# Optimization experiments

Hardware: AMD Instinct MI355X
Metric: run time of the kernel (lower is better)

## Reference

```python
import jax, jax.numpy as jnp
import numpy as np

N_NODES = 100000
N_EDGES = 1600000
LATENT = 64
NODE_DIM = 7
EDGE_DIM = 3
N_PARAMS = 2

def asinh_layer(p, x):
    # learned asinh: a*arcsinh(b*x + c) + d, p = [a, b, c, d]
    return p[0] * jnp.arcsinh(p[1] * x + p[2]) + p[3]

def mlp2(x, w1, b1, w2, b2):
    # ExplicitMLP([L, L]): gelu between layers, none on last
    return jax.nn.gelu(x @ w1 + b1) @ w2 + b2

def agg_stats(x, n):
    # custom_aggregation: [sum, mean, var, max]; mean/var denominators are n_data
    s = jnp.sum(x, axis=0, keepdims=True)
    m = s / n
    v = jnp.sum((x - m) ** 2, axis=0, keepdims=True) / n
    mx = jnp.max(x, axis=0, keepdims=True)
    return jnp.concatenate([s, m, v, mx], axis=-1)

def _forward(nodes, edges, asinh_node, w_en, b_en, asinh_edge, w_ee, b_ee, asinh_glob, w_eg, b_eg, ew1, eb1, ew2, eb2, nw1, nb1, nw2, nb2, gw1, gb1, gw2, gb2, gw3, gb3, senders):
    # decorate_nodes=False -> zero columns 0:4
    nodes = nodes.at[:, 0:4].set(0.0)
    # globals = arcsinh([n_node, n_edge]) as (1, 2)
    glob = jnp.arcsinh(jnp.array([[float(N_NODES), float(N_EDGES)]], dtype=nodes.dtype))
    # GraphMapFeatures embedding: asinh layer + Dense for nodes/edges/globals
    nodes = asinh_layer(asinh_node, nodes) @ w_en + b_en   # (N, L)
    edges = asinh_layer(asinh_edge, edges) @ w_ee + b_ee   # (E, L)
    glob = asinh_layer(asinh_glob, glob) @ w_eg + b_eg     # (1, L)
    # source overwrites receivers with senders
    recv = senders
    # edge update: concat(edges, nodes[senders], nodes[receivers], globals)
    ge = jnp.broadcast_to(glob, (edges.shape[0], glob.shape[-1]))
    e_in = jnp.concatenate([edges, nodes[senders], nodes[recv], ge], axis=-1)  # (E, 4L)
    edges = mlp2(e_in, ew1, eb1, ew2, eb2)                                     # (E, L)
    # node update: sent/received aggregates are identical since recv == senders
    sent = jax.ops.segment_sum(edges, senders, num_segments=N_NODES)           # (N, L)
    gn = jnp.broadcast_to(glob, (nodes.shape[0], glob.shape[-1]))
    n_in = jnp.concatenate([nodes, sent, sent, gn], axis=-1)                   # (N, 4L)
    nodes = mlp2(n_in, nw1, nb1, nw2, nb2)                                     # (N, L)
    # global update: arcsinh of [sum, mean, var, max] over nodes and edges (single graph)
    node_attr = jnp.arcsinh(agg_stats(nodes, float(N_NODES)))                  # (1, 4L)
    edge_attr = jnp.arcsinh(agg_stats(edges, float(N_EDGES)))                  # (1, 4L)
    g_in = jnp.concatenate([node_attr, edge_attr, glob], axis=-1)              # (1, 9L)
    g = jax.nn.gelu(g_in @ gw1 + gb1)
    g = jax.nn.gelu(g @ gw2 + gb2)
    g = g @ gw3 + gb3
    return g.reshape(-1)  # (N_PARAMS,)

def setup_inputs():
    key = jax.random.key(0)
    ks = jax.random.split(key, 16)
    L = LATENT
    def dense(k, fi, fo):
        return jax.random.normal(k, (fi, fo), jnp.float32) / np.float32(np.sqrt(fi))
    z = lambda n: jnp.zeros((n,), jnp.float32)
    asinh0 = jnp.array([1.0, 1.0, 0.0, 0.0], jnp.float32)
    return {
        "nodes": jax.random.normal(ks[0], (N_NODES, NODE_DIM), jnp.float32),
        "edges": jax.random.normal(ks[1], (N_EDGES, EDGE_DIM), jnp.float32),
        "senders": jax.random.randint(ks[2], (N_EDGES,), 0, N_NODES),
        "asinh_node": asinh0, "w_en": dense(ks[3], NODE_DIM, L), "b_en": z(L),
        "asinh_edge": asinh0, "w_ee": dense(ks[4], EDGE_DIM, L), "b_ee": z(L),
        "asinh_glob": asinh0, "w_eg": dense(ks[5], 2, L), "b_eg": z(L),
        "ew1": dense(ks[6], 4 * L, L), "eb1": z(L),
        "ew2": dense(ks[7], L, L), "eb2": z(L),
        "nw1": dense(ks[8], 4 * L, L), "nb1": z(L),
        "nw2": dense(ks[9], L, L), "nb2": z(L),
        "gw1": dense(ks[10], 9 * L, L), "gb1": z(L),
        "gw2": dense(ks[11], L, L), "gb2": z(L),
        "gw3": dense(ks[12], L, N_PARAMS), "gb3": z(N_PARAMS),
    }

def reference(nodes, edges, senders, asinh_node, w_en, b_en, asinh_edge, w_ee, b_ee, asinh_glob, w_eg, b_eg, ew1, eb1, ew2, eb2, nw1, nb1, nw2, nb2, gw1, gb1, gw2, gb2, gw3, gb3):
    return _forward(nodes, edges, asinh_node, w_en, b_en, asinh_edge, w_ee, b_ee, asinh_glob, w_eg, b_eg, ew1, eb1, ew2, eb2, nw1, nb1, nw2, nb2, gw1, gb1, gw2, gb2, gw3, gb3, senders)
```

## Files before the change

kernel.cpp:

```cpp
#include <hip/hip_runtime.h>
#include <cstdint>
#include <cstddef>

#define NN 100000
#define NE 1600000
#define NSLICE 16
#define NBLK 782
#define NBUCK 391
#define CHA 4096
#define CAPB 6144

#define PRE_GLOB 0
#define PRE_WC   64
#define PRE_CVEC 256
#define PRE_CN   320
#define PRE_NGV  384
#define PRE_WSR  448
#define PRE_NSR  4544

#define TAB_W2  0
#define TAB_NW1 1
#define TAB_NSR 2
#define TAB_NW2 3
#define TAB_WSR 4

typedef short v8s __attribute__((ext_vector_type(8)));
typedef float v4f __attribute__((ext_vector_type(4)));

__device__ __forceinline__ float asinhf_fast(float x){
    float ax = fabsf(x);
    float r = __logf(ax + sqrtf(fmaf(ax, ax, 1.0f)));
    return copysignf(r, x);
}
__device__ __forceinline__ float gelu_f(float x){
    float x3 = x * x * x;
    float y = 1.5957691216057308f * fmaf(0.044715f, x3, x);
    float e = __expf(y);
    float r = __builtin_amdgcn_rcpf(e + 1.0f);
    return fmaf(-x, r, x);
}
__device__ __forceinline__ unsigned fkey(float f){
    unsigned u = __float_as_uint(f);
    return (u & 0x80000000u) ? ~u : (u | 0x80000000u);
}
__device__ __forceinline__ float funkey(unsigned k){
    unsigned u = (k & 0x80000000u) ? (k ^ 0x80000000u) : ~k;
    return __uint_as_float(u);
}
__device__ __forceinline__ void atomAddF(float* p, float v){
#if defined(__HIP_DEVICE_COMPILE__)
    unsafeAtomicAdd(p, v);
#else
    atomicAdd(p, v);
#endif
}
__device__ __forceinline__ void split8(const float* x, v8s& hi, v8s& lo){
#pragma unroll
    for (int j = 0; j < 8; ++j){
        unsigned u = __float_as_uint(x[j]);
        float hf = __uint_as_float(u & 0xFFFF0000u);
        float r = x[j] - hf;
        hi[j] = (short)(u >> 16);
        lo[j] = (short)(__float_as_uint(r) >> 16);
    }
}
__device__ __forceinline__ v4f mfma3(v8s ah, v8s al, v8s bh, v8s bl, v4f acc){
    acc = __builtin_amdgcn_mfma_f32_16x16x32_bf16(al, bh, acc, 0, 0, 0);
    acc = __builtin_amdgcn_mfma_f32_16x16x32_bf16(ah, bl, acc, 0, 0, 0);
    acc = __builtin_amdgcn_mfma_f32_16x16x32_bf16(ah, bh, acc, 0, 0, 0);
    return acc;
}
__device__ __forceinline__ void fma16(float acc[4][4], float4 a, float4 b){
    float av[4] = {a.x, a.y, a.z, a.w};
    float bv[4] = {b.x, b.y, b.z, b.w};
#pragma unroll
    for (int i = 0; i < 4; ++i)
#pragma unroll
        for (int c = 0; c < 4; ++c)
            acc[i][c] = fmaf(av[i], bv[c], acc[i][c]);
}

__global__ __launch_bounds__(256) void k_pre(const float* an, const float* w_en, const float* b_en,
                      const float* ae, const float* w_ee, const float* b_ee,
                      const float* ag, const float* w_eg, const float* b_eg,
                      const float* ew1, const float* eb1,
                      const float* nw1, const float* nb1,
                      const float* ew2, const float* nw2,
                      float* pre, unsigned short* preB, int* statsZero, int* counts)
{
    __shared__ float gls[64];
    __shared__ float red[3][4][64];
    __shared__ float redc[4][64], redn[4][64];
    int t = threadIdx.x, col = t & 63, qd = t >> 6;
    for (int i = t; i < 2 * NSLICE * 192; i += 256) statsZero[i] = 0;
    {
        int4* c4 = (int4*)counts;
        int4 z = make_int4(0, 0, 0, 0);
        for (int i = t; i < NN / 4; i += 256) c4[i] = z;
    }
    for (int i = t; i < 4096; i += 256){
        pre[PRE_WSR + i] = ew1[4096 + i] + ew1[8192 + i];
        pre[PRE_NSR + i] = nw1[4096 + i] + nw1[8192 + i];
    }
    if (t < 64){
        float g0 = asinhf_fast(100000.0f);
        float g1 = asinhf_fast(1600000.0f);
        float tg0 = fmaf(ag[0], asinhf_fast(fmaf(ag[1], g0, ag[2])), ag[3]);
        float tg1 = fmaf(ag[0], asinhf_fast(fmaf(ag[1], g1, ag[2])), ag[3]);
        float gl = fmaf(tg0, w_eg[t], fmaf(tg1, w_eg[64 + t], b_eg[t]));
        pre[PRE_GLOB + t] = gl;
        gls[t] = gl;
        float tz = fmaf(an[0], asinhf_fast(an[2]), an[3]);
        pre[PRE_CN + t] = fmaf(tz, w_en[t] + w_en[64 + t] + w_en[128 + t] + w_en[192 + t], b_en[t]);
    }
    __syncthreads();
    {
        float s0 = 0.f, s1 = 0.f, s2 = 0.f, sc = 0.f, sn = 0.f;
        int jb = qd * 16;
#pragma unroll 4
        for (int j = jb; j < jb + 16; ++j){
            float e1 = ew1[j * 64 + col];
            s0 = fmaf(w_ee[j], e1, s0);
            s1 = fmaf(w_ee[64 + j], e1, s1);
            s2 = fmaf(w_ee[128 + j], e1, s2);
            sc = fmaf(b_ee[j], e1, sc);
            float g = gls[j];
            sc = fmaf(g, ew1[(192 + j) * 64 + col], sc);
            sn = fmaf(g, nw1[(192 + j) * 64 + col], sn);
        }
        red[0][qd][col] = s0; red[1][qd][col] = s1; red[2][qd][col] = s2;
        redc[qd][col] = sc; redn[qd][col] = sn;
    }
    __syncthreads();
    if (t < 64){
#pragma unroll
        for (int i = 0; i < 3; ++i)
            pre[PRE_WC + i * 64 + t] = (red[i][0][t] + red[i][1][t]) + (red[i][2][t] + red[i][3][t]);
        pre[PRE_CVEC + t] = eb1[t] + (redc[0][t] + redc[1][t]) + (redc[2][t] + redc[3][t]);
        pre[PRE_NGV + t] = nb1[t] + (redn[0][t] + redn[1][t]) + (redn[2][t] + redn[3][t]);
    }
    __syncthreads();
    const float* srcs[5] = {ew2, nw1, pre + PRE_NSR, nw2, pre + PRE_WSR};
    for (int idx = t; idx < 5 * 4096; idx += 256){
        int tab = idx >> 12;
        int rem = idx & 4095;
        int c = rem >> 10;
        int ch = (rem >> 9) & 1;
        int lane = (rem >> 3) & 63;
        int j = rem & 7;
        int k = ch * 32 + (lane >> 4) * 8 + j;
        int n = c * 16 + (lane & 15);
        float v = srcs[tab][k * 64 + n];
        unsigned u = __float_as_uint(v);
        float hf = __uint_as_float(u & 0xFFFF0000u);
        float r = v - hf;
        int base = tab * 8192 + ((c * 2 + ch) * 2) * 512 + lane * 8 + j;
        preB[base] = (unsigned short)(u >> 16);
        preB[base + 512] = (unsigned short)(__float_as_uint(r) >> 16);
    }
}

__global__ __launch_bounds__(256) void k_nproj(const float* nodes, const float* an,
                                               const float* w_en, const float* pre,
                                               const unsigned short* preB,
                                               const int* senders, int* counts,
                                               float* lat, float* nproj)
{
    __shared__ float fz[64][4];
    __shared__ float latS[64][68];
    int t = threadIdx.x;
    int base = blockIdx.x * 64;
    int cnt = NN - base; if (cnt > 64) cnt = 64;
    {
        const int NT = 1563 * 256;
        for (int i = blockIdx.x * 256 + t; i < NE; i += NT)
            atomicAdd(&counts[senders[i]], 1);
    }
    if (t < 64){
        float pa = an[0], pb = an[1], pc = an[2], pd = an[3];
        int n = base + t;
        float t4 = 0.f, t5 = 0.f, t6 = 0.f;
        if (t < cnt){
            const float* row = nodes + (size_t)n * 7;
            t4 = fmaf(pa, asinhf_fast(fmaf(pb, row[4], pc)), pd);
            t5 = fmaf(pa, asinhf_fast(fmaf(pb, row[5], pc)), pd);
            t6 = fmaf(pa, asinhf_fast(fmaf(pb, row[6], pc)), pd);
        }
        fz[t][0] = t4; fz[t][1] = t5; fz[t][2] = t6;
    }
    __syncthreads();
    {
        int k = t & 63, grp = t >> 6;
        float w4 = w_en[4 * 64 + k], w5 = w_en[5 * 64 + k], w6 = w_en[6 * 64 + k];
        float cn = pre[PRE_CN + k];
#pragma unroll
        for (int i = 0; i < 16; ++i){
            int nl = grp * 16 + i;
            float v = 0.f;
            if (nl < cnt){
                v = cn;
                v = fmaf(fz[nl][0], w4, v);
                v = fmaf(fz[nl][1], w5, v);
                v = fmaf(fz[nl][2], w6, v);
                lat[(size_t)(base + nl) * 64 + k] = v;
            }
            latS[nl][k] = v;
        }
    }
    __syncthreads();
    int l = t & 63, w = t >> 6;
    int m = l & 15, q = l >> 4;
    v8s ah[2], al[2];
#pragma unroll
    for (int ch = 0; ch < 2; ++ch){
        float a[8];
        const float* src = &latS[w * 16 + m][ch * 32 + q * 8];
#pragma unroll
        for (int j = 0; j < 8; ++j) a[j] = src[j];
        split8(a, ah[ch], al[ch]);
    }
    const v8s* WB = (const v8s*)(preB + TAB_WSR * 8192);
    v4f acc[4];
#pragma unroll
    for (int c = 0; c < 4; ++c){
        acc[c] = (v4f){0.f, 0.f, 0.f, 0.f};
#pragma unroll
        for (int ch = 0; ch < 2; ++ch){
            v8s bh = WB[((c * 2 + ch) * 2 + 0) * 64 + l];
            v8s bl = WB[((c * 2 + ch) * 2 + 1) * 64 + l];
            acc[c] = mfma3(ah[ch], al[ch], bh, bl, acc[c]);
        }
    }
#pragma unroll
    for (int c = 0; c < 4; ++c)
#pragma unroll
        for (int r = 0; r < 4; ++r){
            int nl = w * 16 + q * 4 + r;
            if (nl < cnt)
                nproj[(size_t)(base + nl) * 64 + c * 16 + m] = acc[c][r];
        }
}

__global__ __launch_bounds__(128) void k_scanA(const int* counts, int* cursor, int* bsums)
{
    __shared__ int sA[128];
    int t = threadIdx.x, b = blockIdx.x;
    int i = b * 128 + t;
    int v = (i < NN) ? counts[i] : 0;
    sA[t] = v;
    __syncthreads();
    for (int off = 1; off < 128; off <<= 1){
        int x = (t >= off) ? sA[t - off] : 0;
        __syncthreads();
        sA[t] += x;
        __syncthreads();
    }
    if (i < NN) cursor[i] = sA[t] - v;
    if (t == 127) bsums[b] = sA[127];
}

__global__ __launch_bounds__(1024) void k_scanB(const int* bsums, int* bpre, int* bucketFill)
{
    __shared__ int sB[1024];
    int t = threadIdx.x;
    int v = (t < NBLK) ? bsums[t] : 0;
    sB[t] = v;
    __syncthreads();
    for (int off = 1; off < 1024; off <<= 1){
        int x = (t >= off) ? sB[t - off] : 0;
        __syncthreads();
        sB[t] += x;
        __syncthreads();
    }
    if (t < NBLK) bpre[t] = sB[t] - v;
    if (t < NBUCK) bucketFill[t] = (t == 0) ? 0 : sB[2 * t - 1];
}

__global__ __launch_bounds__(256) void k_binA(const int* senders, int* bucketFill, int* binned)
{
    __shared__ int hist[NBUCK], hist2[NBUCK], runS[NBUCK];
    __shared__ int lofs[NBUCK + 1];
    __shared__ int sA[512];
    __shared__ int staged[CHA];
    int t = threadIdx.x, b = blockIdx.x;
    int beg = b * CHA;
    int end = beg + CHA; if (end > NE) end = NE;
    int n = end - beg;
    for (int i = t; i < NBUCK; i += 256){ hist[i] = 0; hist2[i] = 0; }
    __syncthreads();
    for (int i = beg + t; i < end; i += 256)
        atomicAdd(&hist[senders[i] >> 8], 1);
    __syncthreads();
    sA[t] = (t < NBUCK) ? hist[t] : 0;
    sA[t + 256] = (t + 256 < NBUCK) ? hist[t + 256] : 0;
    __syncthreads();
    for (int off = 1; off < 512; off <<= 1){
        int x0 = (t >= off) ? sA[t - off] : 0;
        int p = t + 256;
        int x1 = (p >= off) ? sA[p - off] : 0;
        __syncthreads();
        sA[t] += x0; sA[p] += x1;
        __syncthreads();
    }
    if (t < NBUCK) lofs[t] = sA[t] - hist[t];
    if (t + 256 < NBUCK) lofs[t + 256] = sA[t + 256] - hist[t + 256];
    if (t == 0) lofs[NBUCK] = n;
    for (int i = t; i < NBUCK; i += 256)
        if (hist[i] > 0) runS[i] = atomicAdd(&bucketFill[i], hist[i]);
    __syncthreads();
    for (int i = beg + t; i < end; i += 256){
        int bk = senders[i] >> 8;
        int r = atomicAdd(&hist2[bk], 1);
        staged[lofs[bk] + r] = i;
    }
    __syncthreads();
    for (int p = t; p < n; p += 256){
        int lo = 0, hi = NBUCK;
        while (hi - lo > 1){
            int mid = (lo + hi) >> 1;
            if (lofs[mid] <= p) lo = mid; else hi = mid;
        }
        binned[runS[lo] + (p - lofs[lo])] = staged[p];
    }
}

__global__ __launch_bounds__(256) void k_binB(const int* binned, const int* senders,
                                              const int* cursor, const int* bpre, int* perm)
{
    __shared__ int cnt256[256];
    __shared__ int staged[CAPB];
    int t = threadIdx.x, b = blockIdx.x;
    int base = bpre[2 * b];
    int end = (b == NBUCK - 1) ? NE : bpre[2 * b + 2];
    int cnt = end - base;
    cnt256[t] = 0;
    __syncthreads();
    if (cnt <= CAPB){
        for (int i = base + t; i < end; i += 256){
            int idx = binned[i];
            int s = senders[idx];
            int r = atomicAdd(&cnt256[s & 255], 1);
            int pos = cursor[s] + bpre[s >> 7] + r;
            staged[pos - base] = idx;
        }
        __syncthreads();
        for (int i = t; i < cnt; i += 256) perm[base + i] = staged[i];
    } else {
        for (int i = base + t; i < end; i += 256){
            int idx = binned[i];
            int s = senders[idx];
            int r = atomicAdd(&cnt256[s & 255], 1);
            perm[cursor[s] + bpre[s >> 7] + r] = idx;
        }
    }
}

__global__ __launch_bounds__(256) void k_edge_sorted(const int* perm, const int* senders,
                                                     const float* edges, const float* nproj,
                                                     const float* pre, const unsigned short* preB,
                                                     const float* ae, const float* eb2,
                                                     float* sent, float* epart)
{
    __shared__ float oS[64][65];
    __shared__ float cWs[256];
    __shared__ int sArr[64];
    int t = threadIdx.x;
    cWs[t] = (t < 64) ? pre[PRE_CVEC + t] : pre[PRE_WC + t - 64];
    int l = t & 63, w = t >> 6;
    int m = l & 15, q = l >> 4;
    int e = w * 16 + m;
    int idx = perm[blockIdx.x * 64 + e];
    int s = senders[idx];
    if (q == 0) sArr[e] = s;
    const float* er = edges + (size_t)idx * 3;
    float f0 = er[0], f1 = er[1], f2 = er[2];
    const float4* npb = (const float4*)(nproj + (size_t)s * 64);
    float4 npv0 = npb[2 * q], npv1 = npb[2 * q + 1];
    float4 npv2 = npb[8 + 2 * q], npv3 = npb[8 + 2 * q + 1];
    float pa = ae[0], pb = ae[1], pc = ae[2], pd = ae[3];
    float t0 = fmaf(pa, asinhf_fast(fmaf(pb, f0, pc)), pd);
    float t1 = fmaf(pa, asinhf_fast(fmaf(pb, f1, pc)), pd);
    float t2 = fmaf(pa, asinhf_fast(fmaf(pb, f2, pc)), pd);
    __syncthreads();
    float npf[2][8] = {{npv0.x, npv0.y, npv0.z, npv0.w, npv1.x, npv1.y, npv1.z, npv1.w},
                       {npv2.x, npv2.y, npv2.z, npv2.w, npv3.x, npv3.y, npv3.z, npv3.w}};
    v8s ah[2], al[2];
#pragma unroll
    for (int ch = 0; ch < 2; ++ch){
        int k0 = ch * 32 + q * 8;
        float h[8];
#pragma unroll
        for (int j = 0; j < 8; ++j){
            int k = k0 + j;
            float hp = cWs[k] + npf[ch][j];
            hp = fmaf(t0, cWs[64 + k], hp);
            hp = fmaf(t1, cWs[128 + k], hp);
            hp = fmaf(t2, cWs[192 + k], hp);
            h[j] = gelu_f(hp);
        }
        split8(h, ah[ch], al[ch]);
    }
    const v8s* WB = (const v8s*)(preB + TAB_W2 * 8192);
#pragma unroll
    for (int c = 0; c < 4; ++c){
        v4f acc = (v4f){0.f, 0.f, 0.f, 0.f};
#pragma unroll
        for (int ch = 0; ch < 2; ++ch){
            v8s bh = WB[((c * 2 + ch) * 2 + 0) * 64 + l];
            v8s bl = WB[((c * 2 + ch) * 2 + 1) * 64 + l];
            acc = mfma3(ah[ch], al[ch], bh, bl, acc);
        }
        float bb = eb2[c * 16 + m];
#pragma unroll
        for (int r = 0; r < 4; ++r)
            oS[w * 16 + q * 4 + r][c * 16 + m] = acc[r] + bb;
    }
    __syncthreads();
    if (w == 0){
        int k = l;
        int cur = sArr[0];
        int jstart = 0;
        float a = 0.f;
        for (int j = 0; j < 64; ++j){
            int sj = sArr[j];
            if (sj != cur){
                float* dst = sent + (size_t)cur * 64 + k;
                if (jstart > 0) *dst = a; else atomAddF(dst, a);
                cur = sj; a = 0.f; jstart = j;
            }
            a += oS[j][k];
        }
        atomAddF(sent + (size_t)cur * 64 + k, a);
    } else if (w == 1){
        int k = l;
        float ssum = 0.f, qsum = 0.f, mmax = -INFINITY;
#pragma unroll 4
        for (int j = 0; j < 64; ++j){
            float v = oS[j][k];
            ssum += v;
            qsum = fmaf(v, v, qsum);
            mmax = fmaxf(mmax, v);
        }
        float* ep = epart + (size_t)(blockIdx.x & (NSLICE - 1)) * 192;
        atomAddF(ep + k, ssum);
        atomAddF(ep + 64 + k, qsum);
        atomicMax((unsigned*)(ep + 128) + k, fkey(mmax));
    }
}

__global__ __launch_bounds__(256) void k_edge_atomic(const float* edges, const int* senders,
                                                     const float* nproj, const float* pre,
                                                     const float* ae, const float* ew2, const float* eb2,
                                                     float* sent, float* epart)
{
    __shared__ float hT[64][68];
    __shared__ int sArr[64];
    int t = threadIdx.x;
    int e = t & 63, kq = t >> 6;
    int eg = blockIdx.x * 64 + e;
    int s = senders[eg];
    if (kq == 0) sArr[e] = s;
    float pa = ae[0], pb = ae[1], pc = ae[2], pd = ae[3];
    const float* erow = edges + (size_t)eg * 3;
    float t0 = fmaf(pa, asinhf_fast(fmaf(pb, erow[0], pc)), pd);
    float t1 = fmaf(pa, asinhf_fast(fmaf(pb, erow[1], pc)), pd);
    float t2 = fmaf(pa, asinhf_fast(fmaf(pb, erow[2], pc)), pd);
    int j0 = kq * 16;
    const float* np = nproj + (size_t)s * 64 + j0;
    float npv[16];
#pragma unroll
    for (int qq = 0; qq < 4; ++qq){
        float4 v = *(const float4*)(np + qq * 4);
        npv[qq * 4 + 0] = v.x; npv[qq * 4 + 1] = v.y; npv[qq * 4 + 2] = v.z; npv[qq * 4 + 3] = v.w;
    }
    const float* Wc = pre + PRE_WC;
    const float* cvec = pre + PRE_CVEC;
#pragma unroll
    for (int jj = 0; jj < 16; ++jj){
        int j = j0 + jj;
        float hp = cvec[j] + npv[jj];
        hp = fmaf(t0, Wc[j], hp);
        hp = fmaf(t1, Wc[64 + j], hp);
        hp = fmaf(t2, Wc[128 + j], hp);
        hT[j][e] = gelu_f(hp);
    }
    __syncthreads();
    int e0 = (t & 15) * 4, k0 = (t >> 4) * 4;
    float acc[4][4];
    {
        float4 bb = *(const float4*)(eb2 + k0);
#pragma unroll
        for (int i = 0; i < 4; ++i){ acc[i][0] = bb.x; acc[i][1] = bb.y; acc[i][2] = bb.z; acc[i][3] = bb.w; }
    }
#pragma unroll 4
    for (int j = 0; j < 64; ++j){
        float4 a = *(const float4*)&hT[j][e0];
        float4 b = *(const float4*)(ew2 + j * 64 + k0);
        fma16(acc, a, b);
    }
#pragma unroll
    for (int i = 0; i < 4; ++i){
        int sv = sArr[e0 + i];
        float* dst = sent + (size_t)sv * 64 + k0;
        atomAddF(dst + 0, acc[i][0]);
        atomAddF(dst + 1, acc[i][1]);
        atomAddF(dst + 2, acc[i][2]);
        atomAddF(dst + 3, acc[i][3]);
    }
    float ps[4], pq[4], pm[4];
#pragma unroll
    for (int c = 0; c < 4; ++c){
        float s0 = acc[0][c], s1 = acc[1][c], s2 = acc[2][c], s3 = acc[3][c];
        ps[c] = (s0 + s1) + (s2 + s3);
        pq[c] = fmaf(s0, s0, fmaf(s1, s1, fmaf(s2, s2, s3 * s3)));
        pm[c] = fmaxf(fmaxf(s0, s1), fmaxf(s2, s3));
    }
#pragma unroll
    for (int msk = 1; msk < 16; msk <<= 1){
#pragma unroll
        for (int c = 0; c < 4; ++c){
            ps[c] += __shfl_xor(ps[c], msk);
            pq[c] += __shfl_xor(pq[c], msk);
            pm[c] = fmaxf(pm[c], __shfl_xor(pm[c], msk));
        }
    }
    float* ep = epart + (size_t)(blockIdx.x & (NSLICE - 1)) * 192;
    if ((t & 15) == 0){
#pragma unroll
        for (int c = 0; c < 4; ++c){
            atomAddF(ep + k0 + c, ps[c]);
            atomAddF(ep + 64 + k0 + c, pq[c]);
            atomicMax((unsigned*)(ep + 128) + k0 + c, fkey(pm[c]));
        }
    }
}

__global__ __launch_bounds__(256) void k_node(const float* lat, const float* sent, const float* pre,
                                              const unsigned short* preB, const float* nb2,
                                              float* npart)
{
    __shared__ float h2S[64][68];
    __shared__ float sS[4][64], qS[4][64], mS[4][64];
    int t = threadIdx.x;
    int base = blockIdx.x * 64;
    int cnt = NN - base; if (cnt > 64) cnt = 64;
    int l = t & 63, w = t >> 6;
    int m = l & 15, q = l >> 4;
    int rowA = w * 16 + m;
    bool vA = rowA < cnt;
    v8s lh[2], ll[2], sh[2], sl[2];
#pragma unroll
    for (int ch = 0; ch < 2; ++ch){
        float a[8] = {0,0,0,0,0,0,0,0}, b[8] = {0,0,0,0,0,0,0,0};
        if (vA){
            const float4* pl = (const float4*)(lat + (size_t)(base + rowA) * 64 + ch * 32 + q * 8);
            const float4* psn = (const float4*)(sent + (size_t)(base + rowA) * 64 + ch * 32 + q * 8);
            float4 a0 = pl[0], a1 = pl[1], b0 = psn[0], b1 = psn[1];
            a[0]=a0.x; a[1]=a0.y; a[2]=a0.z; a[3]=a0.w; a[4]=a1.x; a[5]=a1.y; a[6]=a1.z; a[7]=a1.w;
            b[0]=b0.x; b[1]=b0.y; b[2]=b0.z; b[3]=b0.w; b[4]=b1.x; b[5]=b1.y; b[6]=b1.z; b[7]=b1.w;
        }
        split8(a, lh[ch], ll[ch]);
        split8(b, sh[ch], sl[ch]);
    }
    const v8s* B1 = (const v8s*)(preB + TAB_NW1 * 8192);
    const v8s* BS = (const v8s*)(preB + TAB_NSR * 8192);
    v4f acc[4];
#pragma unroll
    for (int c = 0; c < 4; ++c){
        acc[c] = (v4f){0.f, 0.f, 0.f, 0.f};
#pragma unroll
        for (int ch = 0; ch < 2; ++ch){
            v8s bh = B1[((c * 2 + ch) * 2 + 0) * 64 + l];
            v8s bl = B1[((c * 2 + ch) * 2 + 1) * 64 + l];
            acc[c] = mfma3(lh[ch], ll[ch], bh, bl, acc[c]);
            v8s ch2 = BS[((c * 2 + ch) * 2 + 0) * 64 + l];
            v8s cl2 = BS[((c * 2 + ch) * 2 + 1) * 64 + l];
            acc[c] = mfma3(sh[ch], sl[ch], ch2, cl2, acc[c]);
        }
        float g = pre[PRE_NGV + c * 16 + m];
#pragma unroll
        for (int r = 0; r < 4; ++r)
            h2S[w * 16 + q * 4 + r][c * 16 + m] = gelu_f(acc[c][r] + g);
    }
    __syncthreads();
    v8s ah[2], al[2];
#pragma unroll
    for (int ch = 0; ch < 2; ++ch){
        float a[8];
        const float* src = &h2S[w * 16 + m][ch * 32 + q * 8];
#pragma unroll
        for (int j = 0; j < 8; ++j) a[j] = src[j];
        split8(a, ah[ch], al[ch]);
    }
    const v8s* B2 = (const v8s*)(preB + TAB_NW2 * 8192);
    float ps[4], pq[4], pm[4];
#pragma unroll
    for (int c = 0; c < 4; ++c){
        v4f a2 = (v4f){0.f, 0.f, 0.f, 0.f};
#pragma unroll
        for (int ch = 0; ch < 2; ++ch){
            v8s bh = B2[((c * 2 + ch) * 2 + 0) * 64 + l];
            v8s bl = B2[((c * 2 + ch) * 2 + 1) * 64 + l];
            a2 = mfma3(ah[ch], al[ch], bh, bl, a2);
        }
        float bb = nb2[c * 16 + m];
        ps[c] = 0.f; pq[c] = 0.f; pm[c] = -INFINITY;
#pragma unroll
        for (int r = 0; r < 4; ++r){
            int nl = w * 16 + q * 4 + r;
            if (nl < cnt){
                float v = a2[r] + bb;
                ps[c] += v;
                pq[c] = fmaf(v, v, pq[c]);
                pm[c] = fmaxf(pm[c], v);
            }
        }
    }
#pragma unroll
    for (int msk = 16; msk <= 32; msk <<= 1){
#pragma unroll
        for (int c = 0; c < 4; ++c){
            ps[c] += __shfl_xor(ps[c], msk);
            pq[c] += __shfl_xor(pq[c], msk);
            pm[c] = fmaxf(pm[c], __shfl_xor(pm[c], msk));
        }
    }
    if (l < 16){
#pragma unroll
        for (int c = 0; c < 4; ++c){
            sS[w][c * 16 + l] = ps[c];
            qS[w][c * 16 + l] = pq[c];
            mS[w][c * 16 + l] = pm[c];
        }
    }
    __syncthreads();
    if (t < 64){
        int k = t;
        float ssum = sS[0][k] + sS[1][k] + sS[2][k] + sS[3][k];
        float qsum = qS[0][k] + qS[1][k] + qS[2][k] + qS[3][k];
        float mmax = fmaxf(fmaxf(mS[0][k], mS[1][k]), fmaxf(mS[2][k], mS[3][k]));
        float* np = npart + (size_t)(blockIdx.x & (NSLICE - 1)) * 192;
        atomAddF(np + k, ssum);
        atomAddF(np + 64 + k, qsum);
        atomicMax((unsigned*)(np + 128) + k, fkey(mmax));
    }
}

__global__ __launch_bounds__(256) void k_final(const float* pre, const float* epart, const float* npart,
                        const float* gw1, const float* gb1, const float* gw2, const float* gb2,
                        const float* gw3, const float* gb3, float* out)
{
    __shared__ float gin[576];
    __shared__ float p1[4][64];
    __shared__ float l1s[64];
    __shared__ float l2s[64];
    int t = threadIdx.x;
    if (t < 64){
        float ns = 0.f, nq = 0.f; unsigned nmk = 0u;
        float es = 0.f, eq = 0.f; unsigned emk = 0u;
        for (int sl = 0; sl < NSLICE; ++sl){
            const float* np = npart + (size_t)sl * 192;
            const float* ep = epart + (size_t)sl * 192;
            ns += np[t]; nq += np[64 + t];
            unsigned a = ((const unsigned*)(np + 128))[t]; if (a > nmk) nmk = a;
            es += ep[t]; eq += ep[64 + t];
            unsigned b = ((const unsigned*)(ep + 128))[t]; if (b > emk) emk = b;
        }
        float mean = ns / 100000.0f;
        float var = nq / 100000.0f - mean * mean;
        gin[t] = asinhf_fast(ns);
        gin[64 + t] = asinhf_fast(mean);
        gin[128 + t] = asinhf_fast(var);
        gin[192 + t] = asinhf_fast(funkey(nmk));
        float meane = es / 1600000.0f;
        float vare = eq / 1600000.0f - meane * meane;
        gin[256 + t] = asinhf_fast(es);
        gin[320 + t] = asinhf_fast(meane);
        gin[384 + t] = asinhf_fast(vare);
        gin[448 + t] = asinhf_fast(funkey(emk));
        gin[512 + t] = pre[PRE_GLOB + t];
    }
    __syncthreads();
    {
        int col = t & 63, qq = t >> 6;
        float a1 = 0.f;
        for (int j = qq * 144; j < qq * 144 + 144; ++j)
            a1 = fmaf(gin[j], gw1[j * 64 + col], a1);
        p1[qq][col] = a1;
    }
    __syncthreads();
    if (t < 64){
        float a = gb1[t] + ((p1[0][t] + p1[1][t]) + (p1[2][t] + p1[3][t]));
        l1s[t] = gelu_f(a);
    }
    __syncthreads();
    if (t < 64){
        float a2 = gb2[t];
        for (int j = 0; j < 64; ++j) a2 = fmaf(l1s[j], gw2[j * 64 + t], a2);
        l2s[t] = gelu_f(a2);
    }
    __syncthreads();
    if (t < 2){
        float s = gb3[t];
        for (int j = 0; j < 64; ++j) s = fmaf(l2s[j], gw3[j * 2 + t], s);
        out[t] = s;
    }
}

extern "C" void kernel_launch(void* const* d_in, const int* in_sizes, int n_in,
                              void* d_out, int out_size, void* d_ws, size_t ws_size,
                              hipStream_t stream)
{
    const float* nodes  = (const float*)d_in[0];
    const float* edges  = (const float*)d_in[1];
    const int*   senders= (const int*)d_in[2];
    const float* an  = (const float*)d_in[3];
    const float* w_en= (const float*)d_in[4];
    const float* b_en= (const float*)d_in[5];
    const float* ae  = (const float*)d_in[6];
    const float* w_ee= (const float*)d_in[7];
    const float* b_ee= (const float*)d_in[8];
    const float* ag  = (const float*)d_in[9];
    const float* w_eg= (const float*)d_in[10];
    const float* b_eg= (const float*)d_in[11];
    const float* ew1 = (const float*)d_in[12];
    const float* eb1 = (const float*)d_in[13];
    const float* ew2 = (const float*)d_in[14];
    const float* eb2 = (const float*)d_in[15];
    const float* nw1 = (const float*)d_in[16];
    const float* nb1 = (const float*)d_in[17];
    const float* nw2 = (const float*)d_in[18];
    const float* nb2 = (const float*)d_in[19];
    const float* gw1 = (const float*)d_in[20];
    const float* gb1 = (const float*)d_in[21];
    const float* gw2 = (const float*)d_in[22];
    const float* gb2 = (const float*)d_in[23];
    const float* gw3 = (const float*)d_in[24];
    const float* gb3 = (const float*)d_in[25];

    char* ws = (char*)d_ws;
    float*  lat   = (float*)(ws);
    float*  nproj = (float*)(ws + 25600000);
    float*  sent  = (float*)(ws + 51200000);
    float*  pre   = (float*)(ws + 76800000);
    unsigned short* preB = (unsigned short*)(ws + 76865536);
    float*  epart = (float*)(ws + 76963840);
    float*  npart = (float*)(ws + 76976128);
    int*    counts= (int*)  (ws + 77000000);
    int*    cursor= (int*)  (ws + 77400000);
    int*    bsums = (int*)  (ws + 77800000);
    int*    bpre  = (int*)  (ws + 77804096);
    int*    perm  = (int*)  (ws + 77810000);
    int*    binned= (int*)  (ws + 84210000);
    int*    bucketFill = (int*)(ws + 90610000);

    const size_t NEED_FAST = 90620000;
    bool fast = (ws_size >= NEED_FAST);

    hipMemsetAsync(sent, 0, (size_t)NN * 64 * sizeof(float), stream);

    hipLaunchKernelGGL(k_pre, dim3(1), dim3(256), 0, stream,
                       an, w_en, b_en, ae, w_ee, b_ee, ag, w_eg, b_eg, ew1, eb1,
                       nw1, nb1, ew2, nw2, pre, preB, (int*)epart, counts);

    if (fast){
        hipLaunchKernelGGL(k_nproj, dim3((NN + 63) / 64), dim3(256), 0, stream,
                           nodes, an, w_en, pre, preB, senders, counts, lat, nproj);
        hipLaunchKernelGGL(k_scanA, dim3(NBLK), dim3(128), 0, stream, counts, cursor, bsums);
        hipLaunchKernelGGL(k_scanB, dim3(1), dim3(1024), 0, stream, bsums, bpre, bucketFill);
        hipLaunchKernelGGL(k_binA, dim3(NBUCK), dim3(256), 0, stream, senders, bucketFill, binned);
        hipLaunchKernelGGL(k_binB, dim3(NBUCK), dim3(256), 0, stream,
                           binned, senders, cursor, bpre, perm);
        hipLaunchKernelGGL(k_edge_sorted, dim3(NE / 64), dim3(256), 0, stream,
                           perm, senders, edges, nproj, pre, preB, ae, eb2, sent, epart);
    } else {
        hipLaunchKernelGGL(k_nproj, dim3((NN + 63) / 64), dim3(256), 0, stream,
                           nodes, an, w_en, pre, preB, senders, cursor, lat, nproj);
        hipLaunchKernelGGL(k_edge_atomic, dim3(NE / 64), dim3(256), 0, stream,
                           edges, senders, nproj, pre, ae, ew2, eb2, sent, epart);
    }

    hipLaunchKernelGGL(k_node, dim3((NN + 63) / 64), dim3(256), 0, stream,
                       lat, sent, pre, preB, nb2, npart);
    hipLaunchKernelGGL(k_final, dim3(1), dim3(256), 0, stream,
                       pre, epart, npart, gw1, gb1, gw2, gb2, gw3, gb3, (float*)d_out);
}
```

Before: 437.2 us.

## Carry transformed edge features through binning and recompute node latents in node kernel

The binning passes now move packed float4 records holding the three asinh-transformed edge features plus the sender id, instead of edge indices. This removes the perm gather, the senders lookup and the random edge-row reads from the edge kernel. The lat buffer is dropped and node latents are recomputed from the raw node rows inside k_node, and the memset of sent is folded into k_nproj as a grid-stride zero loop. In exchange, binned traffic is four times wider, the workspace requirement grows, and binB loses its shared-memory staging, so its scattered writes now go straight to global memory.

```diff
diff --git a/kernel.cpp b/kernel.cpp
--- a/kernel.cpp
+++ b/kernel.cpp
@@ -7,8 +7,8 @@
 #define NSLICE 16
 #define NBLK 782
 #define NBUCK 391
+#define NCHUNK 391
 #define CHA 4096
-#define CAPB 6144
 
 #define PRE_GLOB 0
 #define PRE_WC   64
@@ -164,24 +164,27 @@
                                                const float* w_en, const float* pre,
                                                const unsigned short* preB,
                                                const int* senders, int* counts,
-                                               float* lat, float* nproj)
+                                               float* sent, float* nproj)
 {
     __shared__ float fz[64][4];
     __shared__ float latS[64][68];
     int t = threadIdx.x;
     int base = blockIdx.x * 64;
     int cnt = NN - base; if (cnt > 64) cnt = 64;
+    const int NT = 1563 * 256;
+    int gtid = blockIdx.x * 256 + t;
+    for (int i = gtid; i < NE; i += NT)
+        atomicAdd(&counts[senders[i]], 1);
     {
-        const int NT = 1563 * 256;
-        for (int i = blockIdx.x * 256 + t; i < NE; i += NT)
-            atomicAdd(&counts[senders[i]], 1);
+        float4 z = make_float4(0.f, 0.f, 0.f, 0.f);
+        float4* s4 = (float4*)sent;
+        for (int i = gtid; i < NN * 16; i += NT) s4[i] = z;
     }
     if (t < 64){
         float pa = an[0], pb = an[1], pc = an[2], pd = an[3];
-        int n = base + t;
         float t4 = 0.f, t5 = 0.f, t6 = 0.f;
         if (t < cnt){
-            const float* row = nodes + (size_t)n * 7;
+            const float* row = nodes + (size_t)(base + t) * 7;
             t4 = fmaf(pa, asinhf_fast(fmaf(pb, row[4], pc)), pd);
             t5 = fmaf(pa, asinhf_fast(fmaf(pb, row[5], pc)), pd);
             t6 = fmaf(pa, asinhf_fast(fmaf(pb, row[6], pc)), pd);
@@ -196,15 +199,11 @@
 #pragma unroll
         for (int i = 0; i < 16; ++i){
             int nl = grp * 16 + i;
-            float v = 0.f;
-            if (nl < cnt){
-                v = cn;
-                v = fmaf(fz[nl][0], w4, v);
-                v = fmaf(fz[nl][1], w5, v);
-                v = fmaf(fz[nl][2], w6, v);
-                lat[(size_t)(base + nl) * 64 + k] = v;
-            }
-            latS[nl][k] = v;
+            float v = cn;
+            v = fmaf(fz[nl][0], w4, v);
+            v = fmaf(fz[nl][1], w5, v);
+            v = fmaf(fz[nl][2], w6, v);
+            latS[nl][k] = (nl < cnt) ? v : 0.f;
         }
     }
     __syncthreads();
@@ -276,7 +275,8 @@
     if (t < NBUCK) bucketFill[t] = (t == 0) ? 0 : sB[2 * t - 1];
 }
 
-__global__ __launch_bounds__(256) void k_binA(const int* senders, int* bucketFill, int* binned)
+__global__ __launch_bounds__(256) void k_binA(const float* edges, const int* senders,
+                                              const float* ae, int* bucketFill, float4* binned)
 {
     __shared__ int hist[NBUCK], hist2[NBUCK], runS[NBUCK];
     __shared__ int lofs[NBUCK + 1];
@@ -314,51 +314,43 @@
         staged[lofs[bk] + r] = i;
     }
     __syncthreads();
+    float pa = ae[0], pb = ae[1], pc = ae[2], pd = ae[3];
     for (int p = t; p < n; p += 256){
         int lo = 0, hi = NBUCK;
         while (hi - lo > 1){
             int mid = (lo + hi) >> 1;
             if (lofs[mid] <= p) lo = mid; else hi = mid;
         }
-        binned[runS[lo] + (p - lofs[lo])] = staged[p];
-    }
-}
-
-__global__ __launch_bounds__(256) void k_binB(const int* binned, const int* senders,
-                                              const int* cursor, const int* bpre, int* perm)
+        int idx = staged[p];
+        const float* er = edges + (size_t)idx * 3;
+        float t0 = fmaf(pa, asinhf_fast(fmaf(pb, er[0], pc)), pd);
+        float t1 = fmaf(pa, asinhf_fast(fmaf(pb, er[1], pc)), pd);
+        float t2 = fmaf(pa, asinhf_fast(fmaf(pb, er[2], pc)), pd);
+        binned[runS[lo] + (p - lofs[lo])] =
+            make_float4(t0, t1, t2, __int_as_float(senders[idx]));
+    }
+}
+
+__global__ __launch_bounds__(256) void k_binB(const float4* binned, const int* cursor,
+                                              const int* bpre, float4* eperm)
 {
     __shared__ int cnt256[256];
-    __shared__ int staged[CAPB];
     int t = threadIdx.x, b = blockIdx.x;
     int base = bpre[2 * b];
     int end = (b == NBUCK - 1) ? NE : bpre[2 * b + 2];
-    int cnt = end - base;
     cnt256[t] = 0;
     __syncthreads();
-    if (cnt <= CAPB){
-        for (int i = base + t; i < end; i += 256){
-            int idx = binned[i];
-            int s = senders[idx];
-            int r = atomicAdd(&cnt256[s & 255], 1);
-            int pos = cursor[s] + bpre[s >> 7] + r;
-            staged[pos - base] = idx;
-        }
-        __syncthreads();
-        for (int i = t; i < cnt; i += 256) perm[base + i] = staged[i];
-    } else {
-        for (int i = base + t; i < end; i += 256){
-            int idx = binned[i];
-            int s = senders[idx];
-            int r = atomicAdd(&cnt256[s & 255], 1);
-            perm[cursor[s] + bpre[s >> 7] + r] = idx;
-        }
-    }
-}
-
-__global__ __launch_bounds__(256) void k_edge_sorted(const int* perm, const int* senders,
-                                                     const float* edges, const float* nproj,
+    for (int i = base + t; i < end; i += 256){
+        float4 ed = binned[i];
+        int s = __float_as_int(ed.w);
+        int r = atomicAdd(&cnt256[s & 255], 1);
+        eperm[cursor[s] + bpre[s >> 7] + r] = ed;
+    }
+}
+
+__global__ __launch_bounds__(256) void k_edge_sorted(const float4* eperm, const float* nproj,
                                                      const float* pre, const unsigned short* preB,
-                                                     const float* ae, const float* eb2,
+                                                     const float* eb2,
                                                      float* sent, float* epart)
 {
     __shared__ float oS[64][65];
@@ -369,18 +361,13 @@
     int l = t & 63, w = t >> 6;
     int m = l & 15, q = l >> 4;
     int e = w * 16 + m;
-    int idx = perm[blockIdx.x * 64 + e];
-    int s = senders[idx];
+    float4 ed = eperm[blockIdx.x * 64 + e];
+    int s = __float_as_int(ed.w);
     if (q == 0) sArr[e] = s;
-    const float* er = edges + (size_t)idx * 3;
-    float f0 = er[0], f1 = er[1], f2 = er[2];
     const float4* npb = (const float4*)(nproj + (size_t)s * 64);
     float4 npv0 = npb[2 * q], npv1 = npb[2 * q + 1];
     float4 npv2 = npb[8 + 2 * q], npv3 = npb[8 + 2 * q + 1];
-    float pa = ae[0], pb = ae[1], pc = ae[2], pd = ae[3];
-    float t0 = fmaf(pa, asinhf_fast(fmaf(pb, f0, pc)), pd);
-    float t1 = fmaf(pa, asinhf_fast(fmaf(pb, f1, pc)), pd);
-    float t2 = fmaf(pa, asinhf_fast(fmaf(pb, f2, pc)), pd);
+    float t0 = ed.x, t1 = ed.y, t2 = ed.z;
     __syncthreads();
     float npf[2][8] = {{npv0.x, npv0.y, npv0.z, npv0.w, npv1.x, npv1.y, npv1.z, npv1.w},
                        {npv2.x, npv2.y, npv2.z, npv2.w, npv3.x, npv3.y, npv3.z, npv3.w}};
@@ -535,28 +522,51 @@
     }
 }
 
-__global__ __launch_bounds__(256) void k_node(const float* lat, const float* sent, const float* pre,
-                                              const unsigned short* preB, const float* nb2,
-                                              float* npart)
-{
+__global__ __launch_bounds__(256) void k_node(const float* nodes, const float* an,
+                                              const float* w_en, const float* sent,
+                                              const float* pre, const unsigned short* preB,
+                                              const float* nb2, float* npart)
+{
+    __shared__ float fz[64][4];
     __shared__ float h2S[64][68];
     __shared__ float sS[4][64], qS[4][64], mS[4][64];
     int t = threadIdx.x;
     int base = blockIdx.x * 64;
     int cnt = NN - base; if (cnt > 64) cnt = 64;
+    if (t < 64){
+        float pa = an[0], pb = an[1], pc = an[2], pd = an[3];
+        float t4 = 0.f, t5 = 0.f, t6 = 0.f;
+        if (t < cnt){
+            const float* row = nodes + (size_t)(base + t) * 7;
+            t4 = fmaf(pa, asinhf_fast(fmaf(pb, row[4], pc)), pd);
+            t5 = fmaf(pa, asinhf_fast(fmaf(pb, row[5], pc)), pd);
+            t6 = fmaf(pa, asinhf_fast(fmaf(pb, row[6], pc)), pd);
+        }
+        fz[t][0] = t4; fz[t][1] = t5; fz[t][2] = t6;
+    }
+    __syncthreads();
     int l = t & 63, w = t >> 6;
     int m = l & 15, q = l >> 4;
     int rowA = w * 16 + m;
     bool vA = rowA < cnt;
+    float f0 = fz[rowA][0], f1 = fz[rowA][1], f2 = fz[rowA][2];
     v8s lh[2], ll[2], sh[2], sl[2];
 #pragma unroll
     for (int ch = 0; ch < 2; ++ch){
-        float a[8] = {0,0,0,0,0,0,0,0}, b[8] = {0,0,0,0,0,0,0,0};
+        int k0 = ch * 32 + q * 8;
+        float a[8], b[8] = {0,0,0,0,0,0,0,0};
+#pragma unroll
+        for (int j = 0; j < 8; ++j){
+            int k = k0 + j;
+            float v = pre[PRE_CN + k];
+            v = fmaf(f0, w_en[4 * 64 + k], v);
+            v = fmaf(f1, w_en[5 * 64 + k], v);
+            v = fmaf(f2, w_en[6 * 64 + k], v);
+            a[j] = vA ? v : 0.f;
+        }
         if (vA){
-            const float4* pl = (const float4*)(lat + (size_t)(base + rowA) * 64 + ch * 32 + q * 8);
-            const float4* psn = (const float4*)(sent + (size_t)(base + rowA) * 64 + ch * 32 + q * 8);
-            float4 a0 = pl[0], a1 = pl[1], b0 = psn[0], b1 = psn[1];
-            a[0]=a0.x; a[1]=a0.y; a[2]=a0.z; a[3]=a0.w; a[4]=a1.x; a[5]=a1.y; a[6]=a1.z; a[7]=a1.w;
+            const float4* psn = (const float4*)(sent + (size_t)(base + rowA) * 64 + k0);
+            float4 b0 = psn[0], b1 = psn[1];
             b[0]=b0.x; b[1]=b0.y; b[2]=b0.z; b[3]=b0.w; b[4]=b1.x; b[5]=b1.y; b[6]=b1.z; b[7]=b1.w;
         }
         split8(a, lh[ch], ll[ch]);
@@ -739,25 +749,22 @@
     const float* gb3 = (const float*)d_in[25];
 
     char* ws = (char*)d_ws;
-    float*  lat   = (float*)(ws);
+    float4* eperm = (float4*)(ws);
     float*  nproj = (float*)(ws + 25600000);
     float*  sent  = (float*)(ws + 51200000);
     float*  pre   = (float*)(ws + 76800000);
     unsigned short* preB = (unsigned short*)(ws + 76865536);
     float*  epart = (float*)(ws + 76963840);
     float*  npart = (float*)(ws + 76976128);
-    int*    counts= (int*)  (ws + 77000000);
-    int*    cursor= (int*)  (ws + 77400000);
-    int*    bsums = (int*)  (ws + 77800000);
-    int*    bpre  = (int*)  (ws + 77804096);
-    int*    perm  = (int*)  (ws + 77810000);
-    int*    binned= (int*)  (ws + 84210000);
-    int*    bucketFill = (int*)(ws + 90610000);
-
-    const size_t NEED_FAST = 90620000;
+    int*    counts= (int*)  (ws + 76988416);
+    int*    cursor= (int*)  (ws + 77388416);
+    int*    bsums = (int*)  (ws + 77788416);
+    int*    bpre  = (int*)  (ws + 77792512);
+    int*    bucketFill = (int*)(ws + 77796608);
+    float4* binned= (float4*)(ws + 77798416);
+
+    const size_t NEED_FAST = 103398416;
     bool fast = (ws_size >= NEED_FAST);
-
-    hipMemsetAsync(sent, 0, (size_t)NN * 64 * sizeof(float), stream);
 
     hipLaunchKernelGGL(k_pre, dim3(1), dim3(256), 0, stream,
                        an, w_en, b_en, ae, w_ee, b_ee, ag, w_eg, b_eg, ew1, eb1,
@@ -765,23 +772,24 @@
 
     if (fast){
         hipLaunchKernelGGL(k_nproj, dim3((NN + 63) / 64), dim3(256), 0, stream,
-                           nodes, an, w_en, pre, preB, senders, counts, lat, nproj);
+                           nodes, an, w_en, pre, preB, senders, counts, sent, nproj);
         hipLaunchKernelGGL(k_scanA, dim3(NBLK), dim3(128), 0, stream, counts, cursor, bsums);
         hipLaunchKernelGGL(k_scanB, dim3(1), dim3(1024), 0, stream, bsums, bpre, bucketFill);
-        hipLaunchKernelGGL(k_binA, dim3(NBUCK), dim3(256), 0, stream, senders, bucketFill, binned);
+        hipLaunchKernelGGL(k_binA, dim3(NCHUNK), dim3(256), 0, stream,
+                           edges, senders, ae, bucketFill, binned);
         hipLaunchKernelGGL(k_binB, dim3(NBUCK), dim3(256), 0, stream,
-                           binned, senders, cursor, bpre, perm);
+                           binned, cursor, bpre, eperm);
         hipLaunchKernelGGL(k_edge_sorted, dim3(NE / 64), dim3(256), 0, stream,
-                           perm, senders, edges, nproj, pre, preB, ae, eb2, sent, epart);
+                           eperm, nproj, pre, preB, eb2, sent, epart);
     } else {
         hipLaunchKernelGGL(k_nproj, dim3((NN + 63) / 64), dim3(256), 0, stream,
-                           nodes, an, w_en, pre, preB, senders, cursor, lat, nproj);
+                           nodes, an, w_en, pre, preB, senders, cursor, sent, nproj);
         hipLaunchKernelGGL(k_edge_atomic, dim3(NE / 64), dim3(256), 0, stream,
                            edges, senders, nproj, pre, ae, ew2, eb2, sent, epart);
     }
 
     hipLaunchKernelGGL(k_node, dim3((NN + 63) / 64), dim3(256), 0, stream,
-                       lat, sent, pre, preB, nb2, npart);
+                       nodes, an, w_en, sent, pre, preB, nb2, npart);
     hipLaunchKernelGGL(k_final, dim3(1), dim3(256), 0, stream,
                        pre, epart, npart, gw1, gb1, gw2, gb2, gw3, gb3, (float*)d_out);
 }
```

After: 429.8 us. Within noise of the previous version (-1.7%).
